# Performance work log

Measured on AMD Instinct MI355X. Metric: run time of the kernel, lower is better.

Reference implementation:

```python
import jax, jax.numpy as jnp
import numpy as np

B, S, HIDDEN = 2, 2048, 2048
N_HEADS, N_KV_HEADS = 32, 8
HEAD_DIM = HIDDEN // N_HEADS          # 64
HALF = HEAD_DIM // 2                  # 32
N_REP = N_HEADS // N_KV_HEADS         # 4
NEG_INF = -1e9


def setup_inputs() -> dict:
    key = jax.random.key(0)
    ks = jax.random.split(key, 5)
    scale = 0.02
    x = jax.random.normal(ks[0], (B, S, HIDDEN), dtype=jnp.float32)
    wq = jax.random.normal(ks[1], (HIDDEN, N_HEADS * HEAD_DIM), dtype=jnp.float32) * scale
    wk = jax.random.normal(ks[2], (HIDDEN, N_KV_HEADS * HEAD_DIM), dtype=jnp.float32) * scale
    wv = jax.random.normal(ks[3], (HIDDEN, N_KV_HEADS * HEAD_DIM), dtype=jnp.float32) * scale
    wo = jax.random.normal(ks[4], (HIDDEN, HIDDEN), dtype=jnp.float32) * scale
    # Llama rotary frequencies: theta = 10000^{-2i/d}, angles = pos * theta
    inv_freq = 1.0 / (10000.0 ** (np.arange(0, HEAD_DIM, 2, dtype=np.float32) / HEAD_DIM))
    angles = np.arange(S, dtype=np.float32)[:, None] * inv_freq[None, :]  # [S, HALF]
    freqs_cos = jnp.asarray(np.cos(angles), dtype=jnp.float32)
    freqs_sin = jnp.asarray(np.sin(angles), dtype=jnp.float32)
    mask = jnp.tril(jnp.ones((S, S), dtype=bool))[None, None]  # causal [1,1,S,S]
    return {"x": x, "wq": wq, "wk": wk, "wv": wv, "wo": wo,
            "freqs_cos": freqs_cos, "freqs_sin": freqs_sin, "mask": mask}


def _apply_rope(t, cos, sin):
    # t: [B, S, H, HEAD_DIM]; cos/sin: [S, HALF] -> broadcast [1, S, 1, HALF]
    tr, ti = t[..., ::2], t[..., 1::2]           # real/imag halves (interleaved pairing)
    c = cos[None, :, None, :]
    s = sin[None, :, None, :]
    out_r = tr * c - ti * s
    out_i = tr * s + ti * c
    out = jnp.stack([out_r, out_i], axis=-1)     # [B,S,H,HALF,2]
    return out.reshape(t.shape)                  # re-interleave


def reference(x, wq, wk, wv, wo, freqs_cos, freqs_sin, mask):
    b, s, _ = x.shape
    xq = (x @ wq).reshape(b, s, N_HEADS, HEAD_DIM)
    xk = (x @ wk).reshape(b, s, N_KV_HEADS, HEAD_DIM)
    xv = (x @ wv).reshape(b, s, N_KV_HEADS, HEAD_DIM)
    xq = _apply_rope(xq, freqs_cos, freqs_sin)
    xk = _apply_rope(xk, freqs_cos, freqs_sin)
    # repeat_kv: interleave-repeat kv heads to match query heads
    xk = jnp.repeat(xk, N_REP, axis=2)           # [B,S,N_HEADS,HEAD_DIM]
    xv = jnp.repeat(xv, N_REP, axis=2)
    q = jnp.transpose(xq, (0, 2, 1, 3))          # [B,H,S,D]
    k = jnp.transpose(xk, (0, 2, 1, 3))
    v = jnp.transpose(xv, (0, 2, 1, 3))
    attn = jnp.einsum('bhqd,bhkd->bhqk', q, k) / jnp.sqrt(jnp.float32(HEAD_DIM))
    attn = attn + (1.0 - mask.astype(attn.dtype)) * NEG_INF  # keras Softmax masking
    attn = jax.nn.softmax(attn, axis=-1)
    out = jnp.einsum('bhqk,bhkd->bhqd', attn, v)
    out = jnp.transpose(out, (0, 2, 1, 3)).reshape(b, s, HIDDEN)
    return out @ wo
```

## Files before the change

### kernel.cpp

```cpp
#include <hip/hip_runtime.h>
#include <cstdint>
#include <cstddef>

#define S_LEN 2048
#define HIDDEN 2048
#define NH 32
#define NKV 8
#define HD 64
#define QKV_W 3072

typedef __bf16 bf16;
typedef __bf16 bf16x8 __attribute__((ext_vector_type(8)));
typedef __bf16 bf16x4 __attribute__((ext_vector_type(4)));
typedef float f32x4 __attribute__((ext_vector_type(4)));
typedef float f32x16 __attribute__((ext_vector_type(16)));

__device__ __forceinline__ void async16(const bf16* g, bf16* l) {
  __builtin_amdgcn_global_load_lds((const __attribute__((address_space(1))) void*)g,
                                   (__attribute__((address_space(3))) void*)l, 16, 0, 0);
}

__global__ void cast_x_kernel(const float* __restrict__ in, bf16* __restrict__ out, int n4) {
  int i = blockIdx.x * blockDim.x + threadIdx.x;
  if (i >= n4) return;
  f32x4 v = ((const f32x4*)in)[i];
  bf16x4 o;
  o[0] = (bf16)v[0]; o[1] = (bf16)v[1]; o[2] = (bf16)v[2]; o[3] = (bf16)v[3];
  ((bf16x4*)out)[i] = o;
}

__global__ void transpose_cast_kernel(const float* __restrict__ in, bf16* __restrict__ out,
                                      int K, int N) {
  __shared__ float tile[32][33];
  const int n0 = blockIdx.x * 32, k0 = blockIdx.y * 32;
  const int tx = threadIdx.x, ty = threadIdx.y;
#pragma unroll
  for (int i = 0; i < 32; i += 8)
    tile[ty + i][tx] = in[(size_t)(k0 + ty + i) * N + n0 + tx];
  __syncthreads();
#pragma unroll
  for (int i = 0; i < 32; i += 8)
    out[(size_t)(n0 + ty + i) * K + k0 + tx] = (bf16)tile[tx][ty + i];
}

template <int MODE>
__global__ __launch_bounds__(256) void gemm_bt_kernel(const bf16* __restrict__ A,
                                                      const bf16* __restrict__ Bt,
                                                      void* __restrict__ Cv,
                                                      int M, int N, int K,
                                                      const float* __restrict__ cosp,
                                                      const float* __restrict__ sinp,
                                                      bf16* __restrict__ vtp) {
  __shared__ bf16 Al[128 * 32];
  __shared__ bf16 Bl[128 * 32];
  const int tid = threadIdx.x;
  const int lane = tid & 63, w = tid >> 6;
  const int quad = lane >> 4, l16 = lane & 15;
  const int m0 = blockIdx.y * 128, n0 = blockIdx.x * 128;
  const int wm = (w >> 1) * 64, wn = (w & 1) * 64;
  f32x4 acc[4][4] = {};
  const int srow = tid >> 2, scol = (tid & 3) * 8;
  const bf16* Ar0 = A + (size_t)(m0 + srow) * K + scol;
  const bf16* Ar1 = A + (size_t)(m0 + 64 + srow) * K + scol;
  const bf16* Br0 = Bt + (size_t)(n0 + srow) * K + scol;
  const bf16* Br1 = Bt + (size_t)(n0 + 64 + srow) * K + scol;
  bf16* al0 = Al + tid * 8;
  bf16* al1 = Al + 2048 + tid * 8;
  bf16* bl0 = Bl + tid * 8;
  bf16* bl1 = Bl + 2048 + tid * 8;
  for (int kt = 0; kt < K; kt += 32) {
    __syncthreads();
    async16(Ar0 + kt, al0);
    async16(Ar1 + kt, al1);
    async16(Br0 + kt, bl0);
    async16(Br1 + kt, bl1);
    __syncthreads();
    bf16x8 a[4], b[4];
#pragma unroll
    for (int mi = 0; mi < 4; ++mi)
      a[mi] = *(const bf16x8*)(Al + (wm + mi * 16 + l16) * 32 + quad * 8);
#pragma unroll
    for (int ni = 0; ni < 4; ++ni)
      b[ni] = *(const bf16x8*)(Bl + (wn + ni * 16 + l16) * 32 + quad * 8);
#pragma unroll
    for (int mi = 0; mi < 4; ++mi)
#pragma unroll
      for (int ni = 0; ni < 4; ++ni)
        acc[mi][ni] = __builtin_amdgcn_mfma_f32_16x16x32_bf16(a[mi], b[ni], acc[mi][ni], 0, 0, 0);
  }
  if (MODE == 0) {
#pragma unroll
    for (int mi = 0; mi < 4; ++mi)
#pragma unroll
      for (int ni = 0; ni < 4; ++ni)
#pragma unroll
        for (int i = 0; i < 4; ++i) {
          const int row = m0 + wm + mi * 16 + quad * 4 + i;
          const int col = n0 + wn + ni * 16 + l16;
          ((float*)Cv)[(size_t)row * N + col] = acc[mi][ni][i];
        }
  } else if (n0 < 2560) {
#pragma unroll
    for (int mi = 0; mi < 4; ++mi)
#pragma unroll
      for (int ni = 0; ni < 4; ++ni)
#pragma unroll
        for (int i = 0; i < 4; ++i) {
          const int row = m0 + wm + mi * 16 + quad * 4 + i;
          const int col = n0 + wn + ni * 16 + l16;
          const float v = acc[mi][ni][i];
          const float p = __shfl_xor(v, 1);
          const int st = row & (S_LEN - 1);
          const int j = (col & 63) >> 1;
          const float cc = cosp[st * 32 + j], ss = sinp[st * 32 + j];
          const float ov = (l16 & 1) ? (p * ss + v * cc) : (v * cc - p * ss);
          ((bf16*)Cv)[(size_t)row * N + col] = (bf16)ov;
        }
  } else {
#pragma unroll
    for (int mi = 0; mi < 4; ++mi)
#pragma unroll
      for (int ni = 0; ni < 4; ++ni) {
        const int col = n0 + wn + ni * 16 + l16;
        const int c = col - 2560;
        const int row0 = m0 + wm + mi * 16 + quad * 4;
        const int batch = row0 >> 11, st0 = row0 & (S_LEN - 1);
        bf16x4 d4;
#pragma unroll
        for (int i = 0; i < 4; ++i) d4[i] = (bf16)acc[mi][ni][i];
        *(bf16x4*)&vtp[((size_t)batch * 512 + c) * S_LEN + st0] = d4;
      }
  }
}

__global__ __launch_bounds__(256) void attn_kernel(const bf16* __restrict__ qkv,
                                                   const bf16* __restrict__ vt,
                                                   bf16* __restrict__ out) {
  __shared__ bf16 Kl[64 * 72];
  __shared__ bf16 Vl[64 * 72];
  __shared__ bf16 Pl[4][32 * 72];
  const int tid = threadIdx.x;
  const int lane = tid & 63, w = tid >> 6;
  const int l32 = lane & 31, half = lane >> 5;
  const int gx = blockIdx.x, h = blockIdx.y, b = blockIdx.z;
  const int kvh = h >> 2;
  const bf16* Kbase = qkv + ((size_t)b * S_LEN) * QKV_W + 2048 + kvh * HD;
  const bf16* vtb = vt + ((size_t)b * 512 + kvh * 64) * S_LEN;
  const int sr = tid >> 3, sc = (tid & 7) * 8;
  bf16* pw = Pl[w];

  for (int pass = 0; pass < 2; ++pass) {
    const int qt = pass ? (15 - gx) : gx;
    const int Q0 = qt * 128;
    const int qw = Q0 + w * 32;
    const int q = qw + l32;
    const bf16* Qrow = qkv + ((size_t)b * S_LEN + q) * QKV_W + h * HD;
    bf16x8 bq[4];
#pragma unroll
    for (int dc = 0; dc < 4; ++dc) bq[dc] = *(const bf16x8*)(Qrow + dc * 16 + half * 8);
    float l_acc = 0.f;
    f32x16 o0 = {}, o1 = {};
    const int ntiles = 2 * qt + 2;
    for (int t = 0; t < ntiles; ++t) {
      const int kt = t * 64;
      __syncthreads();
      *(bf16x8*)&Kl[sr * 72 + sc]        = *(const bf16x8*)(Kbase + (size_t)(kt + sr) * QKV_W + sc);
      *(bf16x8*)&Kl[(sr + 32) * 72 + sc] = *(const bf16x8*)(Kbase + (size_t)(kt + sr + 32) * QKV_W + sc);
      *(bf16x8*)&Vl[sr * 72 + sc]        = *(const bf16x8*)(vtb + (size_t)sr * S_LEN + kt + sc);
      *(bf16x8*)&Vl[(sr + 32) * 72 + sc] = *(const bf16x8*)(vtb + (size_t)(sr + 32) * S_LEN + kt + sc);
      __syncthreads();
      if (kt > qw + 31) continue;
      f32x16 s0 = {}, s1 = {};
#pragma unroll
      for (int dc = 0; dc < 4; ++dc) {
        const bf16x8 ak0 = *(const bf16x8*)&Kl[l32 * 72 + dc * 16 + half * 8];
        const bf16x8 ak1 = *(const bf16x8*)&Kl[(32 + l32) * 72 + dc * 16 + half * 8];
        s0 = __builtin_amdgcn_mfma_f32_32x32x16_bf16(ak0, bq[dc], s0, 0, 0, 0);
        s1 = __builtin_amdgcn_mfma_f32_32x32x16_bf16(ak1, bq[dc], s1, 0, 0, 0);
      }
      const bool needMask = (kt + 63 > qw);
#pragma unroll
      for (int ks = 0; ks < 2; ++ks) {
        const f32x16 sv = ks ? s1 : s0;
#pragma unroll
        for (int r = 0; r < 4; ++r) {
          bf16x4 pv;
#pragma unroll
          for (int c = 0; c < 4; ++c) {
            float p = __expf(fmaf(sv[r * 4 + c], 0.125f, -4.0f));
            const int key = kt + ks * 32 + 8 * r + 4 * half + c;
            if (needMask && key > q) p = 0.f;
            l_acc += p;
            pv[c] = (bf16)p;
          }
          *(bf16x4*)&pw[l32 * 72 + ks * 32 + 8 * r + 4 * half] = pv;
        }
      }
      bf16x8 bp[4];
#pragma unroll
      for (int kc = 0; kc < 4; ++kc) bp[kc] = *(const bf16x8*)&pw[l32 * 72 + kc * 16 + half * 8];
#pragma unroll
      for (int kc = 0; kc < 4; ++kc) {
        const bf16x8 av0 = *(const bf16x8*)&Vl[l32 * 72 + kc * 16 + half * 8];
        const bf16x8 av1 = *(const bf16x8*)&Vl[(32 + l32) * 72 + kc * 16 + half * 8];
        o0 = __builtin_amdgcn_mfma_f32_32x32x16_bf16(av0, bp[kc], o0, 0, 0, 0);
        o1 = __builtin_amdgcn_mfma_f32_32x32x16_bf16(av1, bp[kc], o1, 0, 0, 0);
      }
    }
    const float lt = l_acc + __shfl_xor(l_acc, 32);
    const float rl = 1.0f / lt;
    bf16* orow = out + ((size_t)b * S_LEN + q) * HIDDEN + h * HD;
#pragma unroll
    for (int dsub = 0; dsub < 2; ++dsub) {
      const f32x16 ov = dsub ? o1 : o0;
#pragma unroll
      for (int r = 0; r < 4; ++r) {
        bf16x4 d4;
#pragma unroll
        for (int c = 0; c < 4; ++c) d4[c] = (bf16)(ov[r * 4 + c] * rl);
        *(bf16x4*)(orow + dsub * 32 + 8 * r + 4 * half) = d4;
      }
    }
  }
}

extern "C" void kernel_launch(void* const* d_in, const int* in_sizes, int n_in,
                              void* d_out, int out_size, void* d_ws, size_t ws_size,
                              hipStream_t stream) {
  const float* x = (const float*)d_in[0];
  const float* wq = (const float*)d_in[1];
  const float* wk = (const float*)d_in[2];
  const float* wv = (const float*)d_in[3];
  const float* wo = (const float*)d_in[4];
  const float* fc = (const float*)d_in[5];
  const float* fs = (const float*)d_in[6];

  char* ws = (char*)d_ws;
  bf16* xb   = (bf16*)(ws);
  bf16* wT   = (bf16*)(ws + 16777216);
  bf16* woT  = (bf16*)(ws + 29360128);
  bf16* qkv  = (bf16*)(ws + 37748736);
  bf16* aout = (bf16*)(ws + 62914560);
  bf16* vt   = (bf16*)(ws + 79691776);

  cast_x_kernel<<<8192, 256, 0, stream>>>(x, xb, 2097152);
  transpose_cast_kernel<<<dim3(64, 64), dim3(32, 8), 0, stream>>>(wq, wT, 2048, 2048);
  transpose_cast_kernel<<<dim3(16, 64), dim3(32, 8), 0, stream>>>(wk, wT + (size_t)2048 * 2048, 2048, 512);
  transpose_cast_kernel<<<dim3(16, 64), dim3(32, 8), 0, stream>>>(wv, wT + (size_t)2560 * 2048, 2048, 512);
  transpose_cast_kernel<<<dim3(64, 64), dim3(32, 8), 0, stream>>>(wo, woT, 2048, 2048);

  gemm_bt_kernel<1><<<dim3(24, 32), 256, 0, stream>>>(xb, wT, (void*)qkv, 4096, 3072, 2048, fc, fs, vt);
  attn_kernel<<<dim3(8, 32, 2), 256, 0, stream>>>(qkv, vt, aout);
  gemm_bt_kernel<0><<<dim3(16, 32), 256, 0, stream>>>(aout, woT, d_out, 4096, 2048, 2048, nullptr, nullptr, nullptr);
}
```

Before: 371.0 us.

## Deepen GEMM K-tile to 64 with XOR-swizzled LDS, unpair attention query tiles

```diff
diff --git a/kernel.cpp b/kernel.cpp
--- a/kernel.cpp
+++ b/kernel.cpp
@@ -51,42 +51,49 @@
                                                       const float* __restrict__ cosp,
                                                       const float* __restrict__ sinp,
                                                       bf16* __restrict__ vtp) {
-  __shared__ bf16 Al[128 * 32];
-  __shared__ bf16 Bl[128 * 32];
+  __shared__ bf16 Al[128 * 64];
+  __shared__ bf16 Bl[128 * 64];
   const int tid = threadIdx.x;
   const int lane = tid & 63, w = tid >> 6;
   const int quad = lane >> 4, l16 = lane & 15;
   const int m0 = blockIdx.y * 128, n0 = blockIdx.x * 128;
   const int wm = (w >> 1) * 64, wn = (w & 1) * 64;
   f32x4 acc[4][4] = {};
-  const int srow = tid >> 2, scol = (tid & 3) * 8;
-  const bf16* Ar0 = A + (size_t)(m0 + srow) * K + scol;
-  const bf16* Ar1 = A + (size_t)(m0 + 64 + srow) * K + scol;
-  const bf16* Br0 = Bt + (size_t)(n0 + srow) * K + scol;
-  const bf16* Br1 = Bt + (size_t)(n0 + 64 + srow) * K + scol;
-  bf16* al0 = Al + tid * 8;
-  bf16* al1 = Al + 2048 + tid * 8;
-  bf16* bl0 = Bl + tid * 8;
-  bf16* bl1 = Bl + 2048 + tid * 8;
-  for (int kt = 0; kt < K; kt += 32) {
-    __syncthreads();
-    async16(Ar0 + kt, al0);
-    async16(Ar1 + kt, al1);
-    async16(Br0 + kt, bl0);
-    async16(Br1 + kt, bl1);
-    __syncthreads();
-    bf16x8 a[4], b[4];
-#pragma unroll
-    for (int mi = 0; mi < 4; ++mi)
-      a[mi] = *(const bf16x8*)(Al + (wm + mi * 16 + l16) * 32 + quad * 8);
+  const int srow = tid >> 3;
+  const int scol = (((tid & 7) ^ (srow & 7))) * 8;
+  const bf16* Ab = A + (size_t)(m0 + srow) * K + scol;
+  const bf16* Bb = Bt + (size_t)(n0 + srow) * K + scol;
+  bf16* alp = Al + tid * 8;
+  bf16* blp = Bl + tid * 8;
+  for (int kt = 0; kt < K; kt += 64) {
+    __syncthreads();
+#pragma unroll
+    for (int j = 0; j < 4; ++j) {
+      async16(Ab + (size_t)(32 * j) * K + kt, alp + j * 2048);
+      async16(Bb + (size_t)(32 * j) * K + kt, blp + j * 2048);
+    }
+    __syncthreads();
+    bf16x8 a[4][2], b[4][2];
+#pragma unroll
+    for (int mi = 0; mi < 4; ++mi)
+#pragma unroll
+      for (int kk = 0; kk < 2; ++kk)
+        a[mi][kk] = *(const bf16x8*)(Al + (wm + mi * 16 + l16) * 64 +
+                                     (((kk << 2) | quad) ^ (l16 & 7)) * 8);
 #pragma unroll
     for (int ni = 0; ni < 4; ++ni)
-      b[ni] = *(const bf16x8*)(Bl + (wn + ni * 16 + l16) * 32 + quad * 8);
-#pragma unroll
-    for (int mi = 0; mi < 4; ++mi)
-#pragma unroll
-      for (int ni = 0; ni < 4; ++ni)
-        acc[mi][ni] = __builtin_amdgcn_mfma_f32_16x16x32_bf16(a[mi], b[ni], acc[mi][ni], 0, 0, 0);
+#pragma unroll
+      for (int kk = 0; kk < 2; ++kk)
+        b[ni][kk] = *(const bf16x8*)(Bl + (wn + ni * 16 + l16) * 64 +
+                                     (((kk << 2) | quad) ^ (l16 & 7)) * 8);
+#pragma unroll
+    for (int kk = 0; kk < 2; ++kk)
+#pragma unroll
+      for (int mi = 0; mi < 4; ++mi)
+#pragma unroll
+        for (int ni = 0; ni < 4; ++ni)
+          acc[mi][ni] = __builtin_amdgcn_mfma_f32_16x16x32_bf16(a[mi][kk], b[ni][kk],
+                                                                acc[mi][ni], 0, 0, 0);
   }
   if (MODE == 0) {
 #pragma unroll
@@ -142,84 +149,81 @@
   const int tid = threadIdx.x;
   const int lane = tid & 63, w = tid >> 6;
   const int l32 = lane & 31, half = lane >> 5;
-  const int gx = blockIdx.x, h = blockIdx.y, b = blockIdx.z;
+  const int qt = blockIdx.x, h = blockIdx.y, b = blockIdx.z;
   const int kvh = h >> 2;
   const bf16* Kbase = qkv + ((size_t)b * S_LEN) * QKV_W + 2048 + kvh * HD;
   const bf16* vtb = vt + ((size_t)b * 512 + kvh * 64) * S_LEN;
   const int sr = tid >> 3, sc = (tid & 7) * 8;
   bf16* pw = Pl[w];
 
-  for (int pass = 0; pass < 2; ++pass) {
-    const int qt = pass ? (15 - gx) : gx;
-    const int Q0 = qt * 128;
-    const int qw = Q0 + w * 32;
-    const int q = qw + l32;
-    const bf16* Qrow = qkv + ((size_t)b * S_LEN + q) * QKV_W + h * HD;
-    bf16x8 bq[4];
-#pragma unroll
-    for (int dc = 0; dc < 4; ++dc) bq[dc] = *(const bf16x8*)(Qrow + dc * 16 + half * 8);
-    float l_acc = 0.f;
-    f32x16 o0 = {}, o1 = {};
-    const int ntiles = 2 * qt + 2;
-    for (int t = 0; t < ntiles; ++t) {
-      const int kt = t * 64;
-      __syncthreads();
-      *(bf16x8*)&Kl[sr * 72 + sc]        = *(const bf16x8*)(Kbase + (size_t)(kt + sr) * QKV_W + sc);
-      *(bf16x8*)&Kl[(sr + 32) * 72 + sc] = *(const bf16x8*)(Kbase + (size_t)(kt + sr + 32) * QKV_W + sc);
-      *(bf16x8*)&Vl[sr * 72 + sc]        = *(const bf16x8*)(vtb + (size_t)sr * S_LEN + kt + sc);
-      *(bf16x8*)&Vl[(sr + 32) * 72 + sc] = *(const bf16x8*)(vtb + (size_t)(sr + 32) * S_LEN + kt + sc);
-      __syncthreads();
-      if (kt > qw + 31) continue;
-      f32x16 s0 = {}, s1 = {};
-#pragma unroll
-      for (int dc = 0; dc < 4; ++dc) {
-        const bf16x8 ak0 = *(const bf16x8*)&Kl[l32 * 72 + dc * 16 + half * 8];
-        const bf16x8 ak1 = *(const bf16x8*)&Kl[(32 + l32) * 72 + dc * 16 + half * 8];
-        s0 = __builtin_amdgcn_mfma_f32_32x32x16_bf16(ak0, bq[dc], s0, 0, 0, 0);
-        s1 = __builtin_amdgcn_mfma_f32_32x32x16_bf16(ak1, bq[dc], s1, 0, 0, 0);
+  const int Q0 = qt * 128;
+  const int qw = Q0 + w * 32;
+  const int q = qw + l32;
+  const bf16* Qrow = qkv + ((size_t)b * S_LEN + q) * QKV_W + h * HD;
+  bf16x8 bq[4];
+#pragma unroll
+  for (int dc = 0; dc < 4; ++dc) bq[dc] = *(const bf16x8*)(Qrow + dc * 16 + half * 8);
+  float l_acc = 0.f;
+  f32x16 o0 = {}, o1 = {};
+  const int ntiles = 2 * qt + 2;
+  for (int t = 0; t < ntiles; ++t) {
+    const int kt = t * 64;
+    __syncthreads();
+    *(bf16x8*)&Kl[sr * 72 + sc]        = *(const bf16x8*)(Kbase + (size_t)(kt + sr) * QKV_W + sc);
+    *(bf16x8*)&Kl[(sr + 32) * 72 + sc] = *(const bf16x8*)(Kbase + (size_t)(kt + sr + 32) * QKV_W + sc);
+    *(bf16x8*)&Vl[sr * 72 + sc]        = *(const bf16x8*)(vtb + (size_t)sr * S_LEN + kt + sc);
+    *(bf16x8*)&Vl[(sr + 32) * 72 + sc] = *(const bf16x8*)(vtb + (size_t)(sr + 32) * S_LEN + kt + sc);
+    __syncthreads();
+    if (kt > qw + 31) continue;
+    f32x16 s0 = {}, s1 = {};
+#pragma unroll
+    for (int dc = 0; dc < 4; ++dc) {
+      const bf16x8 ak0 = *(const bf16x8*)&Kl[l32 * 72 + dc * 16 + half * 8];
+      const bf16x8 ak1 = *(const bf16x8*)&Kl[(32 + l32) * 72 + dc * 16 + half * 8];
+      s0 = __builtin_amdgcn_mfma_f32_32x32x16_bf16(ak0, bq[dc], s0, 0, 0, 0);
+      s1 = __builtin_amdgcn_mfma_f32_32x32x16_bf16(ak1, bq[dc], s1, 0, 0, 0);
+    }
+    const bool needMask = (kt + 63 > qw);
+#pragma unroll
+    for (int ks = 0; ks < 2; ++ks) {
+      const f32x16 sv = ks ? s1 : s0;
+#pragma unroll
+      for (int r = 0; r < 4; ++r) {
+        bf16x4 pv;
+#pragma unroll
+        for (int c = 0; c < 4; ++c) {
+          float p = __expf(fmaf(sv[r * 4 + c], 0.125f, -4.0f));
+          const int key = kt + ks * 32 + 8 * r + 4 * half + c;
+          if (needMask && key > q) p = 0.f;
+          l_acc += p;
+          pv[c] = (bf16)p;
+        }
+        *(bf16x4*)&pw[l32 * 72 + ks * 32 + 8 * r + 4 * half] = pv;
       }
-      const bool needMask = (kt + 63 > qw);
-#pragma unroll
-      for (int ks = 0; ks < 2; ++ks) {
-        const f32x16 sv = ks ? s1 : s0;
-#pragma unroll
-        for (int r = 0; r < 4; ++r) {
-          bf16x4 pv;
-#pragma unroll
-          for (int c = 0; c < 4; ++c) {
-            float p = __expf(fmaf(sv[r * 4 + c], 0.125f, -4.0f));
-            const int key = kt + ks * 32 + 8 * r + 4 * half + c;
-            if (needMask && key > q) p = 0.f;
-            l_acc += p;
-            pv[c] = (bf16)p;
-          }
-          *(bf16x4*)&pw[l32 * 72 + ks * 32 + 8 * r + 4 * half] = pv;
-        }
-      }
-      bf16x8 bp[4];
-#pragma unroll
-      for (int kc = 0; kc < 4; ++kc) bp[kc] = *(const bf16x8*)&pw[l32 * 72 + kc * 16 + half * 8];
-#pragma unroll
-      for (int kc = 0; kc < 4; ++kc) {
-        const bf16x8 av0 = *(const bf16x8*)&Vl[l32 * 72 + kc * 16 + half * 8];
-        const bf16x8 av1 = *(const bf16x8*)&Vl[(32 + l32) * 72 + kc * 16 + half * 8];
-        o0 = __builtin_amdgcn_mfma_f32_32x32x16_bf16(av0, bp[kc], o0, 0, 0, 0);
-        o1 = __builtin_amdgcn_mfma_f32_32x32x16_bf16(av1, bp[kc], o1, 0, 0, 0);
-      }
-    }
-    const float lt = l_acc + __shfl_xor(l_acc, 32);
-    const float rl = 1.0f / lt;
-    bf16* orow = out + ((size_t)b * S_LEN + q) * HIDDEN + h * HD;
-#pragma unroll
-    for (int dsub = 0; dsub < 2; ++dsub) {
-      const f32x16 ov = dsub ? o1 : o0;
-#pragma unroll
-      for (int r = 0; r < 4; ++r) {
-        bf16x4 d4;
-#pragma unroll
-        for (int c = 0; c < 4; ++c) d4[c] = (bf16)(ov[r * 4 + c] * rl);
-        *(bf16x4*)(orow + dsub * 32 + 8 * r + 4 * half) = d4;
-      }
+    }
+    bf16x8 bp[4];
+#pragma unroll
+    for (int kc = 0; kc < 4; ++kc) bp[kc] = *(const bf16x8*)&pw[l32 * 72 + kc * 16 + half * 8];
+#pragma unroll
+    for (int kc = 0; kc < 4; ++kc) {
+      const bf16x8 av0 = *(const bf16x8*)&Vl[l32 * 72 + kc * 16 + half * 8];
+      const bf16x8 av1 = *(const bf16x8*)&Vl[(32 + l32) * 72 + kc * 16 + half * 8];
+      o0 = __builtin_amdgcn_mfma_f32_32x32x16_bf16(av0, bp[kc], o0, 0, 0, 0);
+      o1 = __builtin_amdgcn_mfma_f32_32x32x16_bf16(av1, bp[kc], o1, 0, 0, 0);
+    }
+  }
+  const float lt = l_acc + __shfl_xor(l_acc, 32);
+  const float rl = 1.0f / lt;
+  bf16* orow = out + ((size_t)b * S_LEN + q) * HIDDEN + h * HD;
+#pragma unroll
+  for (int dsub = 0; dsub < 2; ++dsub) {
+    const f32x16 ov = dsub ? o1 : o0;
+#pragma unroll
+    for (int r = 0; r < 4; ++r) {
+      bf16x4 d4;
+#pragma unroll
+      for (int c = 0; c < 4; ++c) d4[c] = (bf16)(ov[r * 4 + c] * rl);
+      *(bf16x4*)(orow + dsub * 32 + 8 * r + 4 * half) = d4;
     }
   }
 }
@@ -250,6 +254,6 @@
   transpose_cast_kernel<<<dim3(64, 64), dim3(32, 8), 0, stream>>>(wo, woT, 2048, 2048);
 
   gemm_bt_kernel<1><<<dim3(24, 32), 256, 0, stream>>>(xb, wT, (void*)qkv, 4096, 3072, 2048, fc, fs, vt);
-  attn_kernel<<<dim3(8, 32, 2), 256, 0, stream>>>(qkv, vt, aout);
+  attn_kernel<<<dim3(16, 32, 2), 256, 0, stream>>>(qkv, vt, aout);
   gemm_bt_kernel<0><<<dim3(16, 32), 256, 0, stream>>>(aout, woT, d_out, 4096, 2048, 2048, nullptr, nullptr, nullptr);
 }
```

New measurement: 379.9 us. +2.4%, slower.
